# Kernel optimization log

Hardware: AMD Instinct MI355X
Metric: run time of the kernel (lower is better)

Reference implementation:

```python
import jax, jax.numpy as jnp
from jax import lax
import numpy as np

B, S, T = 256, 1024, 96  # batch, seq_len, tag_size (incl. <BOS>, <EOS>)
START_TAG, STOP_TAG = T - 2, T - 1


def setup_inputs() -> dict:
    key = jax.random.key(0)
    k1, k2, k3, k4 = jax.random.split(key, 4)
    features = jax.random.normal(k1, (B, S, T), dtype=jnp.float32)
    lengths = jax.random.randint(k2, (B,), S // 2, S + 1)
    mask = (jnp.arange(S)[None, :] < lengths[:, None])  # (B,S) bool, prefix mask
    y = jax.random.randint(k3, (B, S), 0, START_TAG).astype(jnp.int64)  # real tags only
    transitions = jax.random.normal(k4, (T, T), dtype=jnp.float32) * 0.1
    return {"features": features, "mask": mask, "y": y, "transitions": transitions}


def _crf_nll(features, mask, y, transitions):
    Bv, Sv, Tv = features.shape
    # ---- log Z via forward algorithm (scan over time) ----
    # scores[t,b,i,j] = features[b,t,j] + transitions[i,j]
    part0 = features[:, 0, :] + transitions[START_TAG, :]  # (B,T) = scores[0,:,START,:]
    feats_t = jnp.swapaxes(features, 0, 1)  # (S,B,T)
    mask_t = jnp.swapaxes(mask, 0, 1)       # (S,B)

    def step(part, inp):
        f_t, m_t = inp  # (B,T), (B,)
        # tmp[b,i,j] = f_t[b,j] + transitions[i,j] + part[b,i]
        tmp = f_t[:, None, :] + transitions[None, :, :] + part[:, :, None]
        new_part = jax.nn.logsumexp(tmp, axis=1)  # (B,T)
        part = jnp.where(m_t[:, None], new_part, part)
        return part, None

    part, _ = lax.scan(step, part0, (feats_t[1:], mask_t[1:]))
    # final transition to STOP, take STOP column of logsumexp over i
    logZ = jnp.sum(jax.nn.logsumexp(part + transitions[:, STOP_TAG][None, :], axis=1))

    # ---- gold score ----
    prev = jnp.concatenate(
        [jnp.full((Bv, 1), START_TAG, dtype=y.dtype), y[:, :-1]], axis=1)  # (B,S)
    emit = jnp.take_along_axis(features, y[:, :, None], axis=2)[:, :, 0]  # features[b,t,y]
    trans = transitions[prev, y]                                          # transitions[prev,y]
    tgt_energy = jnp.sum(jnp.where(mask, emit + trans, 0.0))
    lengths = mask.sum(axis=1)
    last_tag = jnp.take_along_axis(y, (lengths - 1)[:, None], axis=1)[:, 0]
    end_energy = jnp.sum(transitions[last_tag, STOP_TAG])
    gold_score = tgt_energy + end_energy
    return logZ - gold_score


def reference(features, mask, y, transitions):
    return _crf_nll(features, mask, y, transitions)
```

## Files before the change

kernel.cpp:

```cpp
#include <hip/hip_runtime.h>
#include <stdint.h>

#define TT 96
#define SS 1024
#define BB 256
#define START_TAG 94
#define STOP_TAG 95
#define LOG2E 1.44269504088896340736f
#define LN2   0.69314718055994530942f

typedef float f32x4v __attribute__((ext_vector_type(4)));
typedef __bf16 bf16x8 __attribute__((ext_vector_type(8)));

#define EF_BYTES   50331648u
#define ABUF_OFF   50331648u
#define ESTART_OFF 50350080u
#define ESTOP_OFF  50356224u
#define WS_NEED    50427904u

union U4B { uint4 u; bf16x8 v; };

static __device__ __forceinline__ uint32_t pk_bf16(float a, float b) {
    uint32_t r;
    asm("v_cvt_pk_bf16_f32 %0, %1, %2" : "=v"(r) : "v"(a), "v"(b));
    return r;
}

#define MFMA(a, b, c) __builtin_amdgcn_mfma_f32_16x16x32_bf16((a), (b), (c), 0, 0, 0)

__global__ __launch_bounds__(256) void prep_consts(const float* __restrict__ tr,
                                                   char* __restrict__ ws) {
    int i = blockIdx.x * 256 + threadIdx.x;
    if (i < 4608) {
        uint32_t* A = (uint32_t*)(ws + ABUF_OFF);
        int tile = i >> 8, rem = i & 255, l = rem >> 2, v = rem & 3;
        int mt = tile / 3, kt = tile - mt * 3;
        int hi = l >> 4, m = 16 * mt + (l & 15);
        int k0 = 32 * kt + 16 * (v >> 1) + 4 * hi + 2 * (v & 1);
        A[i] = pk_bf16(expf(tr[k0 * TT + m]), expf(tr[(k0 + 1) * TT + m]));
    } else if (i < 4608 + 2 * 1536) {
        int e = i - 4608;
        int stop = (e >= 1536) ? 1 : 0;
        if (stop) e -= 1536;
        int l = e / 24, c = e % 24;
        int mt = c >> 2, r = c & 3, hi = l >> 4;
        int j = 16 * mt + 4 * hi + r;
        float* dst = (float*)(ws + (stop ? ESTOP_OFF : ESTART_OFF));
        dst[e] = expf(stop ? tr[j * TT + STOP_TAG] : tr[START_TAG * TT + j]);
    }
}

__global__ __launch_bounds__(256) void ef_kernel(const float* __restrict__ f,
                                                 uint32_t* __restrict__ ef) {
    int tid  = blockIdx.x * 256 + threadIdx.x;
    int q    = tid % 12;
    int rest = tid / 12;
    int l    = rest & 63;
    int bt   = rest >> 6;
    int t    = bt & 1023;
    int blk  = bt >> 10;
    int b    = blk * 16 + (l & 15);
    int j0   = 16 * (q >> 1) + 4 * (l >> 4) + 2 * (q & 1);
    const float2* p = reinterpret_cast<const float2*>(f + (size_t)(b * SS + t) * TT + j0);
    float2 v = *p;
    ef[tid] = pk_bf16(expf(v.x), expf(v.y));
}

__global__ __launch_bounds__(64, 1) void fwd_kernel(
    const float* __restrict__ features, const int* __restrict__ mask,
    const int* __restrict__ y, const float* __restrict__ trans,
    const char* __restrict__ ws, float* __restrict__ out)
{
    const int l = threadIdx.x;

    if (blockIdx.x >= 16) {
        int bg = blockIdx.x - 16;
        float e = 0.f;
        #pragma unroll 1
        for (int k = 0; k < 18; ++k) {
            int idx = bg * 64 + l + k * 15360;
            if (idx < BB * SS) {
                int t = idx & (SS - 1);
                if (mask[idx]) {
                    int yt   = y[idx];
                    int prev = t ? y[idx - 1] : START_TAG;
                    e += features[(size_t)idx * TT + yt] + trans[prev * TT + yt];
                    bool last = (t == SS - 1) || (mask[idx + 1] == 0);
                    if (last) e += trans[yt * TT + STOP_TAG];
                }
            }
        }
        #pragma unroll
        for (int d = 1; d < 64; d <<= 1) e += __shfl_xor(e, d);
        if (l == 0) atomicAdd(out, -e);
        return;
    }

    const int blk = blockIdx.x;
    const int n = l & 15, hi = l >> 4;

    uint4 efr[8][3];
    const char* efp[8];
    {
        const char* base = ws + ((size_t)(blk * SS) * 64 + l) * 48;
        #pragma unroll
        for (int u = 0; u < 8; ++u) {
            const char* p = base + (size_t)u * 3072;
            efr[u][0] = *(const uint4*)(p);
            efr[u][1] = *(const uint4*)(p + 16);
            efr[u][2] = *(const uint4*)(p + 32);
            efp[u] = p + 8 * 3072;
        }
    }

    int cnt = 0;
    {
        const int4* mrow = (const int4*)(mask + (blk * 16 + n) * SS + 512 + hi * 128);
        #pragma unroll
        for (int k = 0; k < 32; ++k) {
            int4 mv = mrow[k];
            cnt += mv.x + mv.y + mv.z + mv.w;
        }
        cnt += __shfl_xor(cnt, 16);
        cnt += __shfl_xor(cnt, 32);
    }
    const int len_m1 = cnt + 512 - 1;

    bf16x8 Af[6][3];
    {
        const uint4* ab = (const uint4*)(ws + ABUF_OFF);
        #pragma unroll
        for (int mt = 0; mt < 6; ++mt)
            #pragma unroll
            for (int kt = 0; kt < 3; ++kt) {
                U4B ub; ub.u = ab[(mt * 3 + kt) * 64 + l];
                Af[mt][kt] = ub.v;
            }
    }
    float est[6][4];
    {
        const float4* es1 = (const float4*)(ws + ESTOP_OFF);
        #pragma unroll
        for (int mt = 0; mt < 6; ++mt) {
            float4 v = es1[l * 6 + mt];
            est[mt][0] = v.x; est[mt][1] = v.y; est[mt][2] = v.z; est[mt][3] = v.w;
        }
    }

    float c2 = 0.f, pend = 1.0f, pe = 0.f, logz = 0.f;
    bf16x8 Bf[3];
    const f32x4v Z4 = {0.f, 0.f, 0.f, 0.f};

#define UNPACK12(CE0, CE1, CE2, EFV) { \
    uint32_t w_[12] = { CE0.x, CE0.y, CE0.z, CE0.w, CE1.x, CE1.y, CE1.z, CE1.w, \
                        CE2.x, CE2.y, CE2.z, CE2.w }; \
    _Pragma("unroll") \
    for (int q_ = 0; q_ < 12; ++q_) { \
        EFV[q_ >> 1][(q_ & 1) * 2]     = __uint_as_float(w_[q_] << 16); \
        EFV[q_ >> 1][(q_ & 1) * 2 + 1] = __uint_as_float(w_[q_] & 0xffff0000u); \
    } }

#define PACKB(AF) { \
    uint32_t wlo_[6], whi_[6]; \
    _Pragma("unroll") \
    for (int mt_ = 0; mt_ < 6; ++mt_) { \
        wlo_[mt_] = pk_bf16(AF[mt_][0], AF[mt_][1]); \
        whi_[mt_] = pk_bf16(AF[mt_][2], AF[mt_][3]); } \
    _Pragma("unroll") \
    for (int kt_ = 0; kt_ < 3; ++kt_) { \
        U4B ub_; ub_.u.x = wlo_[2 * kt_]; ub_.u.y = whi_[2 * kt_]; \
        ub_.u.z = wlo_[2 * kt_ + 1]; ub_.u.w = whi_[2 * kt_ + 1]; \
        Bf[kt_] = ub_.v; } }

    {
        float esr[6][4];
        const float4* es0 = (const float4*)(ws + ESTART_OFF);
        #pragma unroll
        for (int mt = 0; mt < 6; ++mt) {
            float4 v = es0[l * 6 + mt];
            esr[mt][0] = v.x; esr[mt][1] = v.y; esr[mt][2] = v.z; esr[mt][3] = v.w;
        }
        float efv[6][4];
        UNPACK12(efr[0][0], efr[0][1], efr[0][2], efv);
        float af0[6][4];
        #pragma unroll
        for (int mt = 0; mt < 6; ++mt)
            #pragma unroll
            for (int r = 0; r < 4; ++r) af0[mt][r] = efv[mt][r] * esr[mt][r];
        PACKB(af0);
    }

#define STEP(u, ARED) { \
    uint4 ce0 = efr[u][0], ce1 = efr[u][1], ce2 = efr[u][2]; \
    { const char* p_ = efp[u]; \
      efr[u][0] = *(const uint4*)(p_); \
      efr[u][1] = *(const uint4*)(p_ + 16); \
      efr[u][2] = *(const uint4*)(p_ + 32); \
      efp[u] = p_ + 24576; } \
    f32x4v acc[6]; \
    _Pragma("unroll") \
    for (int mt_ = 0; mt_ < 6; ++mt_) { \
        acc[mt_] = MFMA(Af[mt_][0], Bf[0], Z4); \
        acc[mt_] = MFMA(Af[mt_][1], Bf[1], acc[mt_]); \
        acc[mt_] = MFMA(Af[mt_][2], Bf[2], acc[mt_]); } \
    if (ARED) { c2 += pe; } \
    float efv[6][4]; \
    UNPACK12(ce0, ce1, ce2, efv); \
    float af[6][4]; \
    _Pragma("unroll") \
    for (int mt_ = 0; mt_ < 6; ++mt_) \
        _Pragma("unroll") \
        for (int r_ = 0; r_ < 4; ++r_) { \
            float a_ = acc[mt_][r_]; \
            if (ARED) a_ *= pend; \
            af[mt_][r_] = a_ * efv[mt_][r_]; } \
    { int cap_ = (len_m1 == tb8 + (u)); \
      if (__any(cap_)) { \
          float d_ = 0.f; \
          _Pragma("unroll") \
          for (int mt_ = 0; mt_ < 6; ++mt_) \
              _Pragma("unroll") \
              for (int r_ = 0; r_ < 4; ++r_) d_ = fmaf(af[mt_][r_], est[mt_][r_], d_); \
          d_ += __shfl_xor(d_, 16); d_ += __shfl_xor(d_, 32); \
          float lz_ = LN2 * (c2 + log2f(d_)); \
          logz = cap_ ? lz_ : logz; } } \
    if (ARED) { \
        float m_[6]; \
        _Pragma("unroll") \
        for (int mt_ = 0; mt_ < 6; ++mt_) \
            m_[mt_] = fmaxf(fmaxf(af[mt_][0], af[mt_][1]), fmaxf(af[mt_][2], af[mt_][3])); \
        float mm_ = fmaxf(fmaxf(fmaxf(m_[0], m_[1]), fmaxf(m_[2], m_[3])), fmaxf(m_[4], m_[5])); \
        mm_ = fmaxf(mm_, __shfl_xor(mm_, 16)); \
        mm_ = fmaxf(mm_, __shfl_xor(mm_, 32)); \
        unsigned eb_ = (__float_as_uint(mm_) >> 23) & 255u; \
        pe = (float)((int)eb_ - 127); \
        pend = __uint_as_float((254u - eb_) << 23); } \
    PACKB(af); }

    int tb8 = 0;
    {
        const char* p_ = efp[0];
        efr[0][0] = *(const uint4*)(p_);
        efr[0][1] = *(const uint4*)(p_ + 16);
        efr[0][2] = *(const uint4*)(p_ + 32);
        efp[0] = p_ + 24576;
    }
    STEP(1, 1) STEP(2, 0) STEP(3, 1) STEP(4, 0)
    STEP(5, 1) STEP(6, 0) STEP(7, 1)
    tb8 = 8;
    #pragma unroll 1
    for (int tb = 1; tb < 128; ++tb, tb8 += 8) {
        STEP(0, 0) STEP(1, 1) STEP(2, 0) STEP(3, 1)
        STEP(4, 0) STEP(5, 1) STEP(6, 0) STEP(7, 1)
    }

    if (l < 16) atomicAdd(out, logz);
#undef STEP
#undef PACKB
#undef UNPACK12
}

__global__ void fb_prep(const float* __restrict__ trans, float* __restrict__ E2T) {
    int idx = blockIdx.x * blockDim.x + threadIdx.x;
    if (idx < TT * TT) {
        int jj = idx / TT, ii = idx % TT;
        E2T[idx] = expf(trans[ii * TT + jj]);
    }
}

__global__ __launch_bounds__(384) void fb_forward(
    const float* __restrict__ features, const int* __restrict__ mask,
    const float* __restrict__ trans, const float* __restrict__ E2T,
    float* __restrict__ out)
{
    const int b    = blockIdx.x;
    const int tid  = threadIdx.x;
    const int j    = tid >> 2;
    const int q    = tid & 3;
    const int lane = tid & 63;
    const int wv   = tid >> 6;

    __shared__ float alpha[2][TT];
    __shared__ float fch[2][16 * TT];
    __shared__ float wred[6];
    __shared__ int   wcnt[6];
    __shared__ int   len_sh;

    int cnt = 0;
    for (int i = tid; i < SS; i += 384) cnt += (mask[b * SS + i] != 0);
    #pragma unroll
    for (int d = 1; d < 64; d <<= 1) cnt += __shfl_xor(cnt, d);
    if (lane == 0) wcnt[wv] = cnt;
    __syncthreads();
    if (tid == 0) {
        int L = 0;
        for (int w = 0; w < 6; ++w) L += wcnt[w];
        len_sh = L;
    }

    float Er[24];
    {
        const float4* ep = reinterpret_cast<const float4*>(E2T + j * TT + q * 24);
        #pragma unroll
        for (int k = 0; k < 6; ++k) {
            float4 e4 = ep[k];
            Er[4*k+0] = e4.x; Er[4*k+1] = e4.y; Er[4*k+2] = e4.z; Er[4*k+3] = e4.w;
        }
    }

    const float* fb = features + (size_t)b * SS * TT;
    float4 r0    = reinterpret_cast<const float4*>(fb)[tid];
    float4 rnext = reinterpret_cast<const float4*>(fb + 16 * TT)[tid];
    reinterpret_cast<float4*>(&fch[0][0])[tid] = r0;
    __syncthreads();
    const int len = len_sh;

    if (q == 0) {
        float p0 = fch[0][j] + trans[START_TAG * TT + j];
        alpha[0][j] = exp2f(p0 * LOG2E);
    }
    __syncthreads();

    float c2 = 0.0f;
    float pending = 1.0f;
    int   pe = 0;

    const int clast = (len - 1) >> 4;
    for (int c = 0; c <= clast; ++c) {
        if (c > 0) {
            reinterpret_cast<float4*>(&fch[c & 1][0])[tid] = rnext;
            int cn = c + 1; if (cn > SS / 16 - 1) cn = SS / 16 - 1;
            rnext = reinterpret_cast<const float4*>(fb + cn * 16 * TT)[tid];
            __syncthreads();
        }
        const int t0   = c * 16;
        const int tbeg = (c == 0) ? 1 : t0;
        int tend = t0 + 16; if (tend > len) tend = len;

        for (int t = tbeg; t < tend; ++t) {
            const float* acur = alpha[(t + 1) & 1];
            const float4* ap = reinterpret_cast<const float4*>(acur + q * 24);
            float sum = 0.0f;
            #pragma unroll
            for (int k = 0; k < 6; ++k) {
                float4 a = ap[k];
                sum = fmaf(Er[4*k+0], a.x, sum);
                sum = fmaf(Er[4*k+1], a.y, sum);
                sum = fmaf(Er[4*k+2], a.z, sum);
                sum = fmaf(Er[4*k+3], a.w, sum);
            }
            sum += __shfl_xor(sum, 1);
            sum += __shfl_xor(sum, 2);

            float f    = fch[c & 1][(t - t0) * TT + j];
            float anew = sum * exp2f(f * LOG2E) * pending;
            c2 += (float)pe; pe = 0; pending = 1.0f;

            if (q == 0) alpha[t & 1][j] = anew;
            if ((t & 3) == 3) {
                float m = anew;
                m = fmaxf(m, __shfl_xor(m, 4));
                m = fmaxf(m, __shfl_xor(m, 8));
                m = fmaxf(m, __shfl_xor(m, 16));
                m = fmaxf(m, __shfl_xor(m, 32));
                if (lane == 0) wred[wv] = m;
            }
            __syncthreads();
            if ((t & 3) == 3) {
                float mv = wred[0];
                #pragma unroll
                for (int w = 1; w < 6; ++w) mv = fmaxf(mv, wred[w]);
                int eb  = (int)((__float_as_uint(mv) >> 23) & 255u);
                pe      = eb - 127;
                pending = __uint_as_float((uint32_t)(254 - eb) << 23);
            }
        }
    }

    float v = 0.0f;
    if (q == 0) v = alpha[(len - 1) & 1][j] * E2T[STOP_TAG * TT + j];
    #pragma unroll
    for (int d = 1; d < 64; d <<= 1) v += __shfl_xor(v, d);
    __syncthreads();
    if (lane == 0) wred[wv] = v;
    __syncthreads();
    if (tid == 0) {
        float tot = 0.0f;
        for (int w = 0; w < 6; ++w) tot += wred[w];
        atomicAdd(out, LN2 * (c2 + log2f(tot)));
    }
}

__global__ void fb_gold(const float* __restrict__ features, const int* __restrict__ mask,
                        const int* __restrict__ y, const float* __restrict__ trans,
                        float* __restrict__ out)
{
    int idx = blockIdx.x * blockDim.x + threadIdx.x;
    float e = 0.0f;
    if (idx < BB * SS) {
        int t = idx % SS;
        if (mask[idx] != 0) {
            int yt   = y[idx];
            int prev = (t == 0) ? START_TAG : y[idx - 1];
            e = features[(size_t)idx * TT + yt] + trans[prev * TT + yt];
            bool is_last = (t == SS - 1) || (mask[idx + 1] == 0);
            if (is_last) e += trans[yt * TT + STOP_TAG];
        }
    }
    #pragma unroll
    for (int d = 1; d < 64; d <<= 1) e += __shfl_xor(e, d);
    __shared__ float ws4[4];
    int lane = threadIdx.x & 63, wv = threadIdx.x >> 6;
    if (lane == 0) ws4[wv] = e;
    __syncthreads();
    if (threadIdx.x == 0) {
        float s = ws4[0] + ws4[1] + ws4[2] + ws4[3];
        atomicAdd(out, -s);
    }
}

extern "C" void kernel_launch(void* const* d_in, const int* in_sizes, int n_in,
                              void* d_out, int out_size, void* d_ws, size_t ws_size,
                              hipStream_t stream) {
    const float* features = (const float*)d_in[0];
    const int*   mask     = (const int*)d_in[1];
    const int*   y        = (const int*)d_in[2];
    const float* trans    = (const float*)d_in[3];
    float*       out      = (float*)d_out;

    hipMemsetAsync(d_out, 0, sizeof(float) * out_size, stream);

    if (ws_size >= WS_NEED) {
        char* ws = (char*)d_ws;
        prep_consts<<<30, 256, 0, stream>>>(trans, ws);
        ef_kernel<<<49152, 256, 0, stream>>>(features, (uint32_t*)ws);
        fwd_kernel<<<256, 64, 0, stream>>>(features, mask, y, trans, ws, out);
    } else {
        float* E2T = (float*)d_ws;
        fb_prep<<<(TT * TT + 255) / 256, 256, 0, stream>>>(trans, E2T);
        fb_forward<<<BB, 384, 0, stream>>>(features, mask, trans, E2T, out);
        fb_gold<<<(BB * SS) / 256, 256, 0, stream>>>(features, mask, y, trans, out);
    }
}
```

Before: 544.4 us.

## Stream exp-feature tiles through an LDS ring via async global-to-LDS loads

The forward recurrence kernel now prefetches per-timestep exp(features) tiles into a 16-slot LDS ring using global_load_lds, eight steps ahead. This replaces the 24 uint4 register buffers, which should free VGPRs and keep memory latency off the serial MFMA chain. The elementwise work is rewritten with packed float2 math. Rescaling by the running max now happens every fourth step instead of every second, and the preprocessing kernel handles four floats per thread with 8-byte stores. In exchange the code relies on manual vmcnt waits, and the rarer rescaling leaves less headroom against overflow.

```diff
diff --git a/kernel.cpp b/kernel.cpp
--- a/kernel.cpp
+++ b/kernel.cpp
@@ -9,6 +9,7 @@
 #define LOG2E 1.44269504088896340736f
 #define LN2   0.69314718055994530942f
 
+typedef float f32x2 __attribute__((ext_vector_type(2)));
 typedef float f32x4v __attribute__((ext_vector_type(4)));
 typedef __bf16 bf16x8 __attribute__((ext_vector_type(8)));
 
@@ -25,8 +26,18 @@
     asm("v_cvt_pk_bf16_f32 %0, %1, %2" : "=v"(r) : "v"(a), "v"(b));
     return r;
 }
+static __device__ __forceinline__ f32x2 pmax2(f32x2 a, f32x2 b) {
+#if __has_builtin(__builtin_elementwise_max)
+    return __builtin_elementwise_max(a, b);
+#else
+    f32x2 r; r.x = fmaxf(a.x, b.x); r.y = fmaxf(a.y, b.y); return r;
+#endif
+}
 
 #define MFMA(a, b, c) __builtin_amdgcn_mfma_f32_16x16x32_bf16((a), (b), (c), 0, 0, 0)
+#define GLD(srcp, dstp) __builtin_amdgcn_global_load_lds( \
+    (const __attribute__((address_space(1))) uint32_t*)(srcp), \
+    (__attribute__((address_space(3))) uint32_t*)(dstp), 16, 0, 0)
 
 __global__ __launch_bounds__(256) void prep_consts(const float* __restrict__ tr,
                                                    char* __restrict__ ws) {
@@ -50,20 +61,23 @@
     }
 }
 
-__global__ __launch_bounds__(256) void ef_kernel(const float* __restrict__ f,
-                                                 uint32_t* __restrict__ ef) {
-    int tid  = blockIdx.x * 256 + threadIdx.x;
-    int q    = tid % 12;
-    int rest = tid / 12;
-    int l    = rest & 63;
-    int bt   = rest >> 6;
-    int t    = bt & 1023;
-    int blk  = bt >> 10;
-    int b    = blk * 16 + (l & 15);
-    int j0   = 16 * (q >> 1) + 4 * (l >> 4) + 2 * (q & 1);
-    const float2* p = reinterpret_cast<const float2*>(f + (size_t)(b * SS + t) * TT + j0);
-    float2 v = *p;
-    ef[tid] = pk_bf16(expf(v.x), expf(v.y));
+__global__ __launch_bounds__(256) void ef_kernel2(const float* __restrict__ f,
+                                                  uint32_t* __restrict__ ef) {
+    int tid = blockIdx.x * 256 + threadIdx.x;
+    int p   = tid % 6;
+    int r   = tid / 6;
+    int l   = r & 63;
+    int bt  = r >> 6;
+    int t   = bt & 1023;
+    int blk = bt >> 10;
+    int b   = blk * 16 + (l & 15);
+    int hi  = l >> 4;
+    const float4* fp = (const float4*)(f + (size_t)(b * SS + t) * TT + 16 * p + 4 * hi);
+    float4 v = *fp;
+    uint2 w;
+    w.x = pk_bf16(expf(v.x), expf(v.y));
+    w.y = pk_bf16(expf(v.z), expf(v.w));
+    *(uint2*)(ef + (size_t)r * 12 + 2 * p) = w;
 }
 
 __global__ __launch_bounds__(64, 1) void fwd_kernel(
@@ -96,26 +110,15 @@
         return;
     }
 
+    __shared__ __align__(16) char ring[16 * 3072];
+    char* ringc = (char*)ring;
+
     const int blk = blockIdx.x;
-    const int n = l & 15, hi = l >> 4;
-
-    uint4 efr[8][3];
-    const char* efp[8];
-    {
-        const char* base = ws + ((size_t)(blk * SS) * 64 + l) * 48;
-        #pragma unroll
-        for (int u = 0; u < 8; ++u) {
-            const char* p = base + (size_t)u * 3072;
-            efr[u][0] = *(const uint4*)(p);
-            efr[u][1] = *(const uint4*)(p + 16);
-            efr[u][2] = *(const uint4*)(p + 32);
-            efp[u] = p + 8 * 3072;
-        }
-    }
+    const int n = l & 15;
 
     int cnt = 0;
     {
-        const int4* mrow = (const int4*)(mask + (blk * 16 + n) * SS + 512 + hi * 128);
+        const int4* mrow = (const int4*)(mask + (blk * 16 + n) * SS + 512 + (l >> 4) * 128);
         #pragma unroll
         for (int k = 0; k < 32; ++k) {
             int4 mv = mrow[k];
@@ -137,35 +140,65 @@
                 Af[mt][kt] = ub.v;
             }
     }
-    float est[6][4];
+    f32x2 estL[6], estH[6];
     {
         const float4* es1 = (const float4*)(ws + ESTOP_OFF);
         #pragma unroll
         for (int mt = 0; mt < 6; ++mt) {
             float4 v = es1[l * 6 + mt];
-            est[mt][0] = v.x; est[mt][1] = v.y; est[mt][2] = v.z; est[mt][3] = v.w;
-        }
-    }
-
-    float c2 = 0.f, pend = 1.0f, pe = 0.f, logz = 0.f;
+            estL[mt].x = v.x; estL[mt].y = v.y;
+            estH[mt].x = v.z; estH[mt].y = v.w;
+        }
+    }
+    f32x2 esrL[6], esrH[6];
+    {
+        const float4* es0 = (const float4*)(ws + ESTART_OFF);
+        #pragma unroll
+        for (int mt = 0; mt < 6; ++mt) {
+            float4 v = es0[l * 6 + mt];
+            esrL[mt].x = v.x; esrL[mt].y = v.y;
+            esrH[mt].x = v.z; esrH[mt].y = v.w;
+        }
+    }
+
+    const char* efg = ws + (size_t)blk * SS * 3072 + l * 16;
+    #pragma unroll
+    for (int s = 0; s < 8; ++s) {
+        const char* sp = efg + s * 3072;
+        char* dp = ringc + s * 3072;
+        GLD(sp, dp); GLD(sp + 1024, dp + 1024); GLD(sp + 2048, dp + 2048);
+    }
+    asm volatile("s_waitcnt vmcnt(0)" ::: "memory");
+
+    uint4 PA[3], PB[3];
+    {
+        const uint4* rp = (const uint4*)(ringc + l * 48);
+        PA[0] = rp[0]; PA[1] = rp[1]; PA[2] = rp[2];
+        const uint4* rq = (const uint4*)(ringc + 3072 + l * 48);
+        PB[0] = rq[0]; PB[1] = rq[1]; PB[2] = rq[2];
+    }
+
+    float c2 = 0.f, pe = 0.f, logz = 0.f;
+    f32x2 pend2; pend2.x = 1.f; pend2.y = 1.f;
     bf16x8 Bf[3];
     const f32x4v Z4 = {0.f, 0.f, 0.f, 0.f};
 
-#define UNPACK12(CE0, CE1, CE2, EFV) { \
-    uint32_t w_[12] = { CE0.x, CE0.y, CE0.z, CE0.w, CE1.x, CE1.y, CE1.z, CE1.w, \
-                        CE2.x, CE2.y, CE2.z, CE2.w }; \
+#define UNPACKP(PBUF, EFP) { \
+    uint32_t w_[12] = { PBUF[0].x, PBUF[0].y, PBUF[0].z, PBUF[0].w, \
+                        PBUF[1].x, PBUF[1].y, PBUF[1].z, PBUF[1].w, \
+                        PBUF[2].x, PBUF[2].y, PBUF[2].z, PBUF[2].w }; \
     _Pragma("unroll") \
     for (int q_ = 0; q_ < 12; ++q_) { \
-        EFV[q_ >> 1][(q_ & 1) * 2]     = __uint_as_float(w_[q_] << 16); \
-        EFV[q_ >> 1][(q_ & 1) * 2 + 1] = __uint_as_float(w_[q_] & 0xffff0000u); \
+        EFP[q_ >> 1][q_ & 1].x = __uint_as_float(w_[q_] << 16); \
+        EFP[q_ >> 1][q_ & 1].y = __uint_as_float(w_[q_] & 0xffff0000u); \
     } }
 
-#define PACKB(AF) { \
+#define PACKB2(AFL, AFH) { \
     uint32_t wlo_[6], whi_[6]; \
     _Pragma("unroll") \
     for (int mt_ = 0; mt_ < 6; ++mt_) { \
-        wlo_[mt_] = pk_bf16(AF[mt_][0], AF[mt_][1]); \
-        whi_[mt_] = pk_bf16(AF[mt_][2], AF[mt_][3]); } \
+        wlo_[mt_] = pk_bf16(AFL[mt_].x, AFL[mt_].y); \
+        whi_[mt_] = pk_bf16(AFH[mt_].x, AFH[mt_].y); } \
     _Pragma("unroll") \
     for (int kt_ = 0; kt_ < 3; ++kt_) { \
         U4B ub_; ub_.u.x = wlo_[2 * kt_]; ub_.u.y = whi_[2 * kt_]; \
@@ -173,91 +206,94 @@
         Bf[kt_] = ub_.v; } }
 
     {
-        float esr[6][4];
-        const float4* es0 = (const float4*)(ws + ESTART_OFF);
+        {
+            const char* sp = efg + 8 * 3072;
+            char* dp = ringc + 8 * 3072;
+            GLD(sp, dp); GLD(sp + 1024, dp + 1024); GLD(sp + 2048, dp + 2048);
+        }
+        f32x2 efp[6][2];
+        UNPACKP(PA, efp);
+        f32x2 afL[6], afH[6];
         #pragma unroll
         for (int mt = 0; mt < 6; ++mt) {
-            float4 v = es0[l * 6 + mt];
-            esr[mt][0] = v.x; esr[mt][1] = v.y; esr[mt][2] = v.z; esr[mt][3] = v.w;
-        }
-        float efv[6][4];
-        UNPACK12(efr[0][0], efr[0][1], efr[0][2], efv);
-        float af0[6][4];
-        #pragma unroll
-        for (int mt = 0; mt < 6; ++mt)
-            #pragma unroll
-            for (int r = 0; r < 4; ++r) af0[mt][r] = efv[mt][r] * esr[mt][r];
-        PACKB(af0);
-    }
-
-#define STEP(u, ARED) { \
-    uint4 ce0 = efr[u][0], ce1 = efr[u][1], ce2 = efr[u][2]; \
-    { const char* p_ = efp[u]; \
-      efr[u][0] = *(const uint4*)(p_); \
-      efr[u][1] = *(const uint4*)(p_ + 16); \
-      efr[u][2] = *(const uint4*)(p_ + 32); \
-      efp[u] = p_ + 24576; } \
+            afL[mt] = efp[mt][0] * esrL[mt];
+            afH[mt] = efp[mt][1] * esrH[mt];
+        }
+        PACKB2(afL, afH);
+        asm volatile("s_waitcnt vmcnt(18)" ::: "memory");
+        const uint4* rp = (const uint4*)(ringc + 2 * 3072 + l * 48);
+        PA[0] = rp[0]; PA[1] = rp[1]; PA[2] = rp[2];
+    }
+
+#define STEP(PBUF, TCUR, APPLY, ARED) { \
+    const int t_ = (TCUR); \
+    { int ts_ = t_ + 8; if (ts_ > 1023) ts_ = 1023; \
+      const char* sp_ = efg + (size_t)ts_ * 3072; \
+      char* dp_ = ringc + ((t_ + 8) & 15) * 3072; \
+      GLD(sp_, dp_); GLD(sp_ + 1024, dp_ + 1024); GLD(sp_ + 2048, dp_ + 2048); } \
     f32x4v acc[6]; \
     _Pragma("unroll") \
     for (int mt_ = 0; mt_ < 6; ++mt_) { \
         acc[mt_] = MFMA(Af[mt_][0], Bf[0], Z4); \
         acc[mt_] = MFMA(Af[mt_][1], Bf[1], acc[mt_]); \
         acc[mt_] = MFMA(Af[mt_][2], Bf[2], acc[mt_]); } \
-    if (ARED) { c2 += pe; } \
-    float efv[6][4]; \
-    UNPACK12(ce0, ce1, ce2, efv); \
-    float af[6][4]; \
+    f32x2 efp[6][2]; \
+    UNPACKP(PBUF, efp); \
+    f32x2 afL[6], afH[6]; \
     _Pragma("unroll") \
-    for (int mt_ = 0; mt_ < 6; ++mt_) \
-        _Pragma("unroll") \
-        for (int r_ = 0; r_ < 4; ++r_) { \
-            float a_ = acc[mt_][r_]; \
-            if (ARED) a_ *= pend; \
-            af[mt_][r_] = a_ * efv[mt_][r_]; } \
-    { int cap_ = (len_m1 == tb8 + (u)); \
+    for (int mt_ = 0; mt_ < 6; ++mt_) { \
+        f32x2 aL_, aH_; \
+        aL_.x = acc[mt_][0]; aL_.y = acc[mt_][1]; \
+        aH_.x = acc[mt_][2]; aH_.y = acc[mt_][3]; \
+        if (APPLY) { aL_ = aL_ * pend2; aH_ = aH_ * pend2; } \
+        afL[mt_] = aL_ * efp[mt_][0]; \
+        afH[mt_] = aH_ * efp[mt_][1]; } \
+    if (APPLY) { c2 += pe; } \
+    asm volatile("s_waitcnt vmcnt(18)" ::: "memory"); \
+    { const uint4* rp_ = (const uint4*)(ringc + ((t_ + 2) & 15) * 3072 + l * 48); \
+      PBUF[0] = rp_[0]; PBUF[1] = rp_[1]; PBUF[2] = rp_[2]; } \
+    PACKB2(afL, afH); \
+    { int cap_ = (len_m1 == t_); \
       if (__any(cap_)) { \
-          float d_ = 0.f; \
+          f32x2 ds_ = afL[0] * estL[0]; \
+          ds_ = ds_ + afH[0] * estH[0]; \
           _Pragma("unroll") \
-          for (int mt_ = 0; mt_ < 6; ++mt_) \
-              _Pragma("unroll") \
-              for (int r_ = 0; r_ < 4; ++r_) d_ = fmaf(af[mt_][r_], est[mt_][r_], d_); \
-          d_ += __shfl_xor(d_, 16); d_ += __shfl_xor(d_, 32); \
-          float lz_ = LN2 * (c2 + log2f(d_)); \
+          for (int mt_ = 1; mt_ < 6; ++mt_) { \
+              ds_ = ds_ + afL[mt_] * estL[mt_]; \
+              ds_ = ds_ + afH[mt_] * estH[mt_]; } \
+          float dd_ = ds_.x + ds_.y; \
+          dd_ += __shfl_xor(dd_, 16); dd_ += __shfl_xor(dd_, 32); \
+          float lz_ = LN2 * (c2 + log2f(dd_)); \
           logz = cap_ ? lz_ : logz; } } \
     if (ARED) { \
-        float m_[6]; \
+        f32x2 mp_ = pmax2(afL[0], afH[0]); \
         _Pragma("unroll") \
-        for (int mt_ = 0; mt_ < 6; ++mt_) \
-            m_[mt_] = fmaxf(fmaxf(af[mt_][0], af[mt_][1]), fmaxf(af[mt_][2], af[mt_][3])); \
-        float mm_ = fmaxf(fmaxf(fmaxf(m_[0], m_[1]), fmaxf(m_[2], m_[3])), fmaxf(m_[4], m_[5])); \
+        for (int mt_ = 1; mt_ < 6; ++mt_) \
+            mp_ = pmax2(mp_, pmax2(afL[mt_], afH[mt_])); \
+        float mm_ = fmaxf(mp_.x, mp_.y); \
         mm_ = fmaxf(mm_, __shfl_xor(mm_, 16)); \
         mm_ = fmaxf(mm_, __shfl_xor(mm_, 32)); \
         unsigned eb_ = (__float_as_uint(mm_) >> 23) & 255u; \
         pe = (float)((int)eb_ - 127); \
-        pend = __uint_as_float((254u - eb_) << 23); } \
-    PACKB(af); }
-
-    int tb8 = 0;
-    {
-        const char* p_ = efp[0];
-        efr[0][0] = *(const uint4*)(p_);
-        efr[0][1] = *(const uint4*)(p_ + 16);
-        efr[0][2] = *(const uint4*)(p_ + 32);
-        efp[0] = p_ + 24576;
-    }
-    STEP(1, 1) STEP(2, 0) STEP(3, 1) STEP(4, 0)
-    STEP(5, 1) STEP(6, 0) STEP(7, 1)
-    tb8 = 8;
+        float pn_ = __uint_as_float((254u - eb_) << 23); \
+        pend2.x = pn_; pend2.y = pn_; } }
+
+    STEP(PB, 1, 1, 0)
+    STEP(PA, 2, 0, 0)
+    STEP(PB, 3, 0, 1)
     #pragma unroll 1
-    for (int tb = 1; tb < 128; ++tb, tb8 += 8) {
-        STEP(0, 0) STEP(1, 1) STEP(2, 0) STEP(3, 1)
-        STEP(4, 0) STEP(5, 1) STEP(6, 0) STEP(7, 1)
+    for (int tb = 1; tb < 256; ++tb) {
+        const int t4 = tb * 4;
+        STEP(PA, t4 + 0, 0, 0)
+        STEP(PB, t4 + 1, 1, 0)
+        STEP(PA, t4 + 2, 0, 0)
+        STEP(PB, t4 + 3, 0, 1)
     }
 
     if (l < 16) atomicAdd(out, logz);
 #undef STEP
-#undef PACKB
-#undef UNPACK12
+#undef PACKB2
+#undef UNPACKP
 }
 
 __global__ void fb_prep(const float* __restrict__ trans, float* __restrict__ E2T) {
@@ -433,7 +469,7 @@
     if (ws_size >= WS_NEED) {
         char* ws = (char*)d_ws;
         prep_consts<<<30, 256, 0, stream>>>(trans, ws);
-        ef_kernel<<<49152, 256, 0, stream>>>(features, (uint32_t*)ws);
+        ef_kernel2<<<24576, 256, 0, stream>>>(features, (uint32_t*)ws);
         fwd_kernel<<<256, 64, 0, stream>>>(features, mask, y, trans, ws, out);
     } else {
         float* E2T = (float*)d_ws;
```

Measured after the change: 538.9 us. Within noise of the previous version (-1.0%).
